# Kernel tuning notes

Hardware: AMD Instinct MI355X
Metric: run time of the kernel (lower is better)

Reference implementation:

```python
import jax, jax.numpy as jnp
import numpy as np
from math import ceil, log2

LEVELS = 10
DB4 = [-0.010597401785069032, 0.0328830116668852, 0.030841381835560764,
       -0.18703481171909309, -0.027983769416859854, 0.6308807679298589,
       0.7148465705529157, 0.2303778133088965]


def _convolve(x, f, transpose=False):
    # circular convolution (or correlation if transpose) via rFFT, filter zero-padded to signal length
    L = x.shape[-1]
    ra = jnp.fft.rfft(x)
    rb = jnp.fft.rfft(f, n=L)
    if transpose:
        rb = jnp.conj(rb)
    return jnp.fft.irfft(ra * rb, n=L)


def _compute_wavelet(s):
    # g = flip(s); g[1::2] *= -1
    g = jnp.flip(s, -1)
    sign = jnp.where(jnp.arange(g.shape[-1]) % 2 == 1, -1.0, 1.0).astype(g.dtype)
    return g * sign


def _compute_wavelet_synthesis(s):
    # g = flip(s); g[::2] *= -1
    g = jnp.flip(s, -1)
    sign = jnp.where(jnp.arange(g.shape[-1]) % 2 == 0, -1.0, 1.0).astype(g.dtype)
    return g * sign


def _hard_threshold(v, alpha, b_plus, b_minus):
    return v * (jax.nn.sigmoid(alpha * (v - b_plus)) + jax.nn.sigmoid(-alpha * (v + b_minus)))


def setup_inputs() -> dict:
    key = jax.random.key(0)
    x = jax.random.normal(key, (256, 65536), dtype=jnp.float32)
    filt = jnp.asarray(DB4, dtype=jnp.float32)
    scaling = jnp.tile(filt, (LEVELS, 1))       # (levels, 8)
    scaling_rec = jnp.tile(filt, (LEVELS, 1))   # (levels, 8)
    alpha = jnp.asarray(10.0, jnp.float32)
    b_plus = jnp.asarray(2.0, jnp.float32)
    b_minus = jnp.asarray(1.0, jnp.float32)
    return {"x": x, "scaling": scaling, "scaling_rec": scaling_rec,
            "alpha": alpha, "b_plus": b_plus, "b_minus": b_minus}


def reference(x, scaling, scaling_rec, alpha, b_plus, b_minus):
    n, input_length = x.shape
    desired = 2 ** ceil(log2(input_length))
    pad_l = (desired - input_length) // 2
    pad_r = ceil((desired - input_length) / 2)
    if pad_l or pad_r:
        x = jnp.pad(x, ((0, 0), (pad_l, pad_r)), mode="reflect")

    # forward lifting: note details = even_updated, new approximation = odd_updated
    approx = x
    coeffs = []
    for lvl in range(LEVELS):
        wav = _compute_wavelet(scaling_rec[lvl])
        even = approx[:, ::2]
        odd = approx[:, 1::2]
        odd_u = odd - _convolve(even, wav)
        even_u = even - _convolve(odd, scaling[lvl])
        coeffs.append(even_u)   # details
        approx = odd_u          # approximation
    coeffs.append(approx)

    filtered = [_hard_threshold(c, alpha, b_plus, b_minus) for c in coeffs]
    # l1_reg on a single tensor is sum(abs(.)) in the original code
    reg_loss = sum(jnp.sum(jnp.abs(c)) for c in filtered)

    # inverse lifting
    approx = filtered[-1]
    for lvl in reversed(range(LEVELS)):
        details = filtered[lvl]
        ws = _compute_wavelet_synthesis(scaling_rec[lvl])
        even, odd = details, approx
        even_rest = even + _convolve(odd, scaling[lvl], transpose=True)
        odd_rest = odd + _convolve(even, ws, transpose=True)
        # interleave even/odd back
        approx = jnp.stack([even_rest, odd_rest], axis=-1).reshape(even.shape[0], even.shape[1] * 2)

    return approx[:, pad_l:input_length + pad_l], reg_loss
```

## Files before the change

kernel.cpp:

```cpp
#include <hip/hip_runtime.h>

#define NROWS 256
#define ROWLEN 65536
#define TPB 1024
#define LOSS_IDX ((size_t)NROWS * (size_t)ROWLEN)

__device__ __forceinline__ int SW(int i) {
    return i ^ (((i >> 5) ^ (i >> 10)) & 31);
}

__device__ __forceinline__ float rfl(float x) {
    union { float f; int i; } u; u.f = x;
    u.i = __builtin_amdgcn_readfirstlane(u.i);
    return u.f;
}

__device__ __forceinline__ float sigm(float z) { return 1.0f / (1.0f + __expf(-z)); }

__device__ __forceinline__ float hthr(float v, float a, float bp, float bm) {
    return v * (sigm(a * (v - bp)) + sigm(-a * (v + bm)));
}

__device__ __forceinline__ void wave_sync() {
    __builtin_amdgcn_wave_barrier();
    __threadfence_block();
    __builtin_amdgcn_wave_barrier();
}

__device__ __forceinline__ void ldf_fwd(const float* sc, const float* rec, int lvl,
                                        float* sf, float* wv) {
    #pragma unroll
    for (int i = 0; i < 8; ++i) sf[i] = rfl(sc[lvl * 8 + i]);
    #pragma unroll
    for (int i = 0; i < 8; ++i) {
        float r = rfl(rec[lvl * 8 + 7 - i]);
        wv[i] = (i & 1) ? -r : r;
    }
}

__device__ __forceinline__ void ldf_rec(const float* sc, const float* rec, int lvl,
                                        float* sf, float* ws) {
    #pragma unroll
    for (int i = 0; i < 8; ++i) sf[i] = rfl(sc[lvl * 8 + i]);
    #pragma unroll
    for (int i = 0; i < 8; ++i) {
        float r = rfl(rec[lvl * 8 + 7 - i]);
        ws[i] = (i & 1) ? r : -r;
    }
}

template<int C, int S, int M, bool WAVE>
__device__ __forceinline__ void fwd_level(float* __restrict__ buf, int tid,
                                          const float* sf, const float* wv,
                                          float a, float bp, float bm, float& loss)
{
    const int c0 = tid * C;
    float ev[8], od[8];
    #pragma unroll
    for (int k = 0; k < 7; ++k) {
        int m = (c0 - 7 + k) & (M - 1);
        ev[k] = buf[SW(2 * m * S)];
        od[k] = buf[SW((2 * m + 1) * S)];
    }
    if constexpr (WAVE) wave_sync(); else __syncthreads();
    float ne = buf[SW(2 * c0 * S)];
    float no = buf[SW((2 * c0 + 1) * S)];
    #pragma unroll
    for (int j = 0; j < C; ++j) {
        const int n = c0 + j;
        ev[7] = ne; od[7] = no;
        if (j + 1 < C) {
            ne = buf[SW(2 * (n + 1) * S)];
            no = buf[SW((2 * (n + 1) + 1) * S)];
        }
        float ao = 0.f, ae = 0.f;
        #pragma unroll
        for (int k = 0; k < 8; ++k) {
            ao = fmaf(wv[k], ev[7 - k], ao);
            ae = fmaf(sf[k], od[7 - k], ae);
        }
        buf[SW(2 * n * S)] = od[7] - ao;
        float d = hthr(ev[7] - ae, a, bp, bm);
        loss += fabsf(d);
        buf[SW((2 * n + 1) * S)] = d;
        #pragma unroll
        for (int k = 0; k < 7; ++k) { ev[k] = ev[k + 1]; od[k] = od[k + 1]; }
    }
    if constexpr (WAVE) wave_sync(); else __syncthreads();
}

template<int C, int S, int M, bool WAVE>
__device__ __forceinline__ void rec_level(float* __restrict__ buf, int tid,
                                          const float* sf, const float* ws)
{
    const int c0 = tid * C;
    float ha[7], hd[7];
    #pragma unroll
    for (int k = 0; k < 7; ++k) {
        int m = (c0 + C + k) & (M - 1);
        ha[k] = buf[SW(2 * m * S)];
        hd[k] = buf[SW((2 * m + 1) * S)];
    }
    if constexpr (WAVE) wave_sync(); else __syncthreads();
    float ap[8], dt[8];
    #pragma unroll
    for (int k = 0; k < 8; ++k) {
        if (k < C) {
            ap[k] = buf[SW(2 * (c0 + k) * S)];
            dt[k] = buf[SW((2 * (c0 + k) + 1) * S)];
        } else {
            ap[k] = ha[k - C];
            dt[k] = hd[k - C];
        }
    }
    #pragma unroll
    for (int j = 0; j < C; ++j) {
        const int n = c0 + j;
        float er = 0.f, orr = 0.f;
        #pragma unroll
        for (int k = 0; k < 8; ++k) {
            er  = fmaf(sf[k], ap[k], er);
            orr = fmaf(ws[k], dt[k], orr);
        }
        er  += dt[0];
        orr += ap[0];
        buf[SW(2 * n * S)] = er;
        buf[SW((2 * n + 1) * S)] = orr;
        if (j + 1 < C) {
            #pragma unroll
            for (int k = 0; k < 7; ++k) { ap[k] = ap[k + 1]; dt[k] = dt[k + 1]; }
            const int nn = n + 8;
            if (j + 8 < C) {
                ap[7] = buf[SW(2 * nn * S)];
                dt[7] = buf[SW((2 * nn + 1) * S)];
            } else {
                ap[7] = ha[j + 8 - C];
                dt[7] = hd[j + 8 - C];
            }
        }
    }
    if constexpr (WAVE) wave_sync(); else __syncthreads();
}

__global__ __launch_bounds__(TPB)
__attribute__((amdgpu_num_vgpr(128), amdgpu_waves_per_eu(4, 4)))
void wavelet_vcycle_kernel(
    const float* __restrict__ x, const float* __restrict__ scaling,
    const float* __restrict__ scaling_rec, const float* __restrict__ pa,
    const float* __restrict__ pbp, const float* __restrict__ pbm,
    float* __restrict__ out)
{
    extern __shared__ float buf[];
    __shared__ float wb[16][8];
    __shared__ float lossbuf[16];
    const int tid  = threadIdx.x;
    const int lane = tid & 63;
    const int wv_id = tid >> 6;
    const int row = blockIdx.x;
    const float* xr = x + (size_t)row * ROWLEN;
    float* outr = out + (size_t)row * ROWLEN;
    const float a = rfl(pa[0]), bp = rfl(pbp[0]), bm = rfl(pbm[0]);
    float loss = 0.f;
    float sf[8], wv8[8];
    float det0[32];

    ldf_fwd(scaling, scaling_rec, 0, sf, wv8);
    {
        const int c0 = tid * 32;
        float ev[8], od[8];
        {
            const int b = 2 * c0;
            float4 h0 = *(const float4*)(xr + ((b - 16) & 65535));
            float4 h1 = *(const float4*)(xr + ((b - 12) & 65535));
            float4 h2 = *(const float4*)(xr + ((b -  8) & 65535));
            float4 h3 = *(const float4*)(xr + ((b -  4) & 65535));
            ev[0] = h0.z; od[0] = h0.w;
            ev[1] = h1.x; od[1] = h1.y; ev[2] = h1.z; od[2] = h1.w;
            ev[3] = h2.x; od[3] = h2.y; ev[4] = h2.z; od[4] = h2.w;
            ev[5] = h3.x; od[5] = h3.y; ev[6] = h3.z; od[6] = h3.w;
        }
        #pragma unroll
        for (int jj = 0; jj < 16; ++jj) {
            float4 v = *(const float4*)(xr + 2 * (c0 + 2 * jj));
            #pragma unroll
            for (int q = 0; q < 2; ++q) {
                const int j = 2 * jj + q;
                const int n = c0 + j;
                ev[7] = (q == 0) ? v.x : v.z;
                od[7] = (q == 0) ? v.y : v.w;
                float ao = 0.f, ae = 0.f;
                #pragma unroll
                for (int k = 0; k < 8; ++k) {
                    ao = fmaf(wv8[k], ev[7 - k], ao);
                    ae = fmaf(sf[k],  od[7 - k], ae);
                }
                buf[SW(n)] = od[7] - ao;
                float d = hthr(ev[7] - ae, a, bp, bm);
                loss += fabsf(d);
                det0[j] = d;
                #pragma unroll
                for (int k = 0; k < 7; ++k) { ev[k] = ev[k + 1]; od[k] = od[k + 1]; }
            }
        }
    }
    if (lane == 0) {
        #pragma unroll
        for (int k = 0; k < 7; ++k) wb[wv_id][k] = det0[k];
    }
    __syncthreads();

    ldf_fwd(scaling, scaling_rec, 1, sf, wv8); fwd_level<16, 1, 16384, false>(buf, tid, sf, wv8, a, bp, bm, loss);
    ldf_fwd(scaling, scaling_rec, 2, sf, wv8); fwd_level< 8, 2,  8192, false>(buf, tid, sf, wv8, a, bp, bm, loss);
    ldf_fwd(scaling, scaling_rec, 3, sf, wv8); fwd_level< 4, 4,  4096, false>(buf, tid, sf, wv8, a, bp, bm, loss);
    ldf_fwd(scaling, scaling_rec, 4, sf, wv8); fwd_level< 2, 8,  2048, false>(buf, tid, sf, wv8, a, bp, bm, loss);

    if (wv_id == 0) {
        ldf_fwd(scaling, scaling_rec, 5, sf, wv8); fwd_level<16,  16, 1024, true>(buf, lane, sf, wv8, a, bp, bm, loss);
        ldf_fwd(scaling, scaling_rec, 6, sf, wv8); fwd_level< 8,  32,  512, true>(buf, lane, sf, wv8, a, bp, bm, loss);
        ldf_fwd(scaling, scaling_rec, 7, sf, wv8); fwd_level< 4,  64,  256, true>(buf, lane, sf, wv8, a, bp, bm, loss);
        ldf_fwd(scaling, scaling_rec, 8, sf, wv8); fwd_level< 2, 128,  128, true>(buf, lane, sf, wv8, a, bp, bm, loss);
        ldf_fwd(scaling, scaling_rec, 9, sf, wv8); fwd_level< 1, 256,   64, true>(buf, lane, sf, wv8, a, bp, bm, loss);

        float v = buf[SW(lane * 512)];
        float f = hthr(v, a, bp, bm);
        loss += fabsf(f);
        buf[SW(lane * 512)] = f;
        wave_sync();

        ldf_rec(scaling, scaling_rec, 9, sf, wv8); rec_level< 1, 256,   64, true>(buf, lane, sf, wv8);
        ldf_rec(scaling, scaling_rec, 8, sf, wv8); rec_level< 2, 128,  128, true>(buf, lane, sf, wv8);
        ldf_rec(scaling, scaling_rec, 7, sf, wv8); rec_level< 4,  64,  256, true>(buf, lane, sf, wv8);
        ldf_rec(scaling, scaling_rec, 6, sf, wv8); rec_level< 8,  32,  512, true>(buf, lane, sf, wv8);
        ldf_rec(scaling, scaling_rec, 5, sf, wv8); rec_level<16,  16, 1024, true>(buf, lane, sf, wv8);
    }

    {
        float l = loss;
        #pragma unroll
        for (int off = 32; off > 0; off >>= 1) l += __shfl_down(l, off, 64);
        if (lane == 0) lossbuf[wv_id] = l;
    }
    __syncthreads();
    if (tid == 0) {
        float s = 0.f;
        #pragma unroll
        for (int w = 0; w < 16; ++w) s += lossbuf[w];
        atomicAdd(out + LOSS_IDX, s);
    }

    ldf_rec(scaling, scaling_rec, 4, sf, wv8); rec_level< 2, 8, 2048, false>(buf, tid, sf, wv8);
    ldf_rec(scaling, scaling_rec, 3, sf, wv8); rec_level< 4, 4, 4096, false>(buf, tid, sf, wv8);
    ldf_rec(scaling, scaling_rec, 2, sf, wv8); rec_level< 8, 2, 8192, false>(buf, tid, sf, wv8);
    ldf_rec(scaling, scaling_rec, 1, sf, wv8); rec_level<16, 1, 16384, false>(buf, tid, sf, wv8);

    {
        ldf_rec(scaling, scaling_rec, 0, sf, wv8);
        float h[7];
        #pragma unroll
        for (int k = 0; k < 7; ++k) h[k] = __shfl(det0[k], (lane + 1) & 63, 64);
        if (lane == 63) {
            #pragma unroll
            for (int k = 0; k < 7; ++k) h[k] = wb[(wv_id + 1) & 15][k];
        }
        #pragma unroll
        for (int p = 0; p < 2; ++p) {
            const int c0 = tid * 32 + p * 16;
            float ap[8];
            #pragma unroll
            for (int k = 0; k < 8; ++k) ap[k] = buf[SW((c0 + k) & 32767)];
            float e0 = 0.f, o0 = 0.f;
            #pragma unroll
            for (int j = 0; j < 16; ++j) {
                const int n = c0 + j;
                float er = 0.f, orr = 0.f;
                #pragma unroll
                for (int k = 0; k < 8; ++k) {
                    const int di = p * 16 + j + k;
                    float dv = (di < 32) ? det0[di] : h[di - 32];
                    er  = fmaf(sf[k],  ap[k], er);
                    orr = fmaf(wv8[k], dv,    orr);
                }
                const int d0i = p * 16 + j;
                float dvj = (d0i < 32) ? det0[d0i] : h[d0i - 32];
                er  += dvj;
                orr += ap[0];
                if ((j & 1) == 0) { e0 = er; o0 = orr; }
                else *(float4*)(outr + 2 * (n - 1)) = make_float4(e0, o0, er, orr);
                if (j < 15) {
                    #pragma unroll
                    for (int k = 0; k < 7; ++k) ap[k] = ap[k + 1];
                    ap[7] = buf[SW((n + 8) & 32767)];
                }
            }
        }
    }
}

extern "C" void kernel_launch(void* const* d_in, const int* in_sizes, int n_in,
                              void* d_out, int out_size, void* d_ws, size_t ws_size,
                              hipStream_t stream) {
    const float* x           = (const float*)d_in[0];
    const float* scaling     = (const float*)d_in[1];
    const float* scaling_rec = (const float*)d_in[2];
    const float* p_alpha     = (const float*)d_in[3];
    const float* p_bp        = (const float*)d_in[4];
    const float* p_bm        = (const float*)d_in[5];
    float* out = (float*)d_out;

    hipMemsetAsync(out + LOSS_IDX, 0, sizeof(float), stream);

    wavelet_vcycle_kernel<<<dim3(NROWS), dim3(TPB), 32768 * sizeof(float), stream>>>(
        x, scaling, scaling_rec, p_alpha, p_bp, p_bm, out);
}
```

Measured before the change: 85.54 us.

## Parallelize levels 5-6 across block, fuse threshold sigmoids, prefetch input loads

Moves wavelet levels 5 and 6 (forward and inverse) from a single wavefront to the whole 1024-thread block, with a guard for level 6 where only half the threads have work. This cuts the serial single-wave tail, at the cost of two extra block-wide barriers per direction. The hard threshold now combines both sigmoids into one expression with a single fast reciprocal, clamping the exponents to avoid overflow. The global input loads for level 0 are software-pipelined four float4s ahead.

New measurement: 73.49 us. 14.1% less time.

```diff
diff --git a/kernel.cpp b/kernel.cpp
--- a/kernel.cpp
+++ b/kernel.cpp
@@ -15,10 +15,13 @@
     return u.f;
 }
 
-__device__ __forceinline__ float sigm(float z) { return 1.0f / (1.0f + __expf(-z)); }
-
 __device__ __forceinline__ float hthr(float v, float a, float bp, float bm) {
-    return v * (sigm(a * (v - bp)) + sigm(-a * (v + bm)));
+    float e1 = __expf(fminf(-a * (v - bp), 80.f));
+    float e2 = __expf(fminf( a * (v + bm), 80.f));
+    float s  = e1 + e2;
+    float num = 2.f + s;
+    float den = fmaf(e1, e2, 1.f + s);
+    return v * num * __builtin_amdgcn_rcpf(den);
 }
 
 __device__ __forceinline__ void wave_sync() {
@@ -49,93 +52,103 @@
     }
 }
 
-template<int C, int S, int M, bool WAVE>
+template<int C, int S, int M, bool WAVE, bool GUARD>
 __device__ __forceinline__ void fwd_level(float* __restrict__ buf, int tid,
                                           const float* sf, const float* wv,
                                           float a, float bp, float bm, float& loss)
 {
+    const bool act = !GUARD || (tid * C < M);
     const int c0 = tid * C;
     float ev[8], od[8];
-    #pragma unroll
-    for (int k = 0; k < 7; ++k) {
-        int m = (c0 - 7 + k) & (M - 1);
-        ev[k] = buf[SW(2 * m * S)];
-        od[k] = buf[SW((2 * m + 1) * S)];
+    if (act) {
+        #pragma unroll
+        for (int k = 0; k < 7; ++k) {
+            int m = (c0 - 7 + k) & (M - 1);
+            ev[k] = buf[SW(2 * m * S)];
+            od[k] = buf[SW((2 * m + 1) * S)];
+        }
     }
     if constexpr (WAVE) wave_sync(); else __syncthreads();
-    float ne = buf[SW(2 * c0 * S)];
-    float no = buf[SW((2 * c0 + 1) * S)];
-    #pragma unroll
-    for (int j = 0; j < C; ++j) {
-        const int n = c0 + j;
-        ev[7] = ne; od[7] = no;
-        if (j + 1 < C) {
-            ne = buf[SW(2 * (n + 1) * S)];
-            no = buf[SW((2 * (n + 1) + 1) * S)];
-        }
-        float ao = 0.f, ae = 0.f;
-        #pragma unroll
-        for (int k = 0; k < 8; ++k) {
-            ao = fmaf(wv[k], ev[7 - k], ao);
-            ae = fmaf(sf[k], od[7 - k], ae);
-        }
-        buf[SW(2 * n * S)] = od[7] - ao;
-        float d = hthr(ev[7] - ae, a, bp, bm);
-        loss += fabsf(d);
-        buf[SW((2 * n + 1) * S)] = d;
-        #pragma unroll
-        for (int k = 0; k < 7; ++k) { ev[k] = ev[k + 1]; od[k] = od[k + 1]; }
+    if (act) {
+        float ne = buf[SW(2 * c0 * S)];
+        float no = buf[SW((2 * c0 + 1) * S)];
+        #pragma unroll
+        for (int j = 0; j < C; ++j) {
+            const int n = c0 + j;
+            ev[7] = ne; od[7] = no;
+            if (j + 1 < C) {
+                ne = buf[SW(2 * (n + 1) * S)];
+                no = buf[SW((2 * (n + 1) + 1) * S)];
+            }
+            float ao = 0.f, ae = 0.f;
+            #pragma unroll
+            for (int k = 0; k < 8; ++k) {
+                ao = fmaf(wv[k], ev[7 - k], ao);
+                ae = fmaf(sf[k], od[7 - k], ae);
+            }
+            buf[SW(2 * n * S)] = od[7] - ao;
+            float d = hthr(ev[7] - ae, a, bp, bm);
+            loss += fabsf(d);
+            buf[SW((2 * n + 1) * S)] = d;
+            #pragma unroll
+            for (int k = 0; k < 7; ++k) { ev[k] = ev[k + 1]; od[k] = od[k + 1]; }
+        }
     }
     if constexpr (WAVE) wave_sync(); else __syncthreads();
 }
 
-template<int C, int S, int M, bool WAVE>
+template<int C, int S, int M, bool WAVE, bool GUARD>
 __device__ __forceinline__ void rec_level(float* __restrict__ buf, int tid,
                                           const float* sf, const float* ws)
 {
+    const bool act = !GUARD || (tid * C < M);
     const int c0 = tid * C;
     float ha[7], hd[7];
-    #pragma unroll
-    for (int k = 0; k < 7; ++k) {
-        int m = (c0 + C + k) & (M - 1);
-        ha[k] = buf[SW(2 * m * S)];
-        hd[k] = buf[SW((2 * m + 1) * S)];
+    if (act) {
+        #pragma unroll
+        for (int k = 0; k < 7; ++k) {
+            int m = (c0 + C + k) & (M - 1);
+            ha[k] = buf[SW(2 * m * S)];
+            hd[k] = buf[SW((2 * m + 1) * S)];
+        }
     }
     if constexpr (WAVE) wave_sync(); else __syncthreads();
-    float ap[8], dt[8];
-    #pragma unroll
-    for (int k = 0; k < 8; ++k) {
-        if (k < C) {
-            ap[k] = buf[SW(2 * (c0 + k) * S)];
-            dt[k] = buf[SW((2 * (c0 + k) + 1) * S)];
-        } else {
-            ap[k] = ha[k - C];
-            dt[k] = hd[k - C];
-        }
-    }
-    #pragma unroll
-    for (int j = 0; j < C; ++j) {
-        const int n = c0 + j;
-        float er = 0.f, orr = 0.f;
+    if (act) {
+        float ap[8], dt[8];
         #pragma unroll
         for (int k = 0; k < 8; ++k) {
-            er  = fmaf(sf[k], ap[k], er);
-            orr = fmaf(ws[k], dt[k], orr);
-        }
-        er  += dt[0];
-        orr += ap[0];
-        buf[SW(2 * n * S)] = er;
-        buf[SW((2 * n + 1) * S)] = orr;
-        if (j + 1 < C) {
-            #pragma unroll
-            for (int k = 0; k < 7; ++k) { ap[k] = ap[k + 1]; dt[k] = dt[k + 1]; }
-            const int nn = n + 8;
-            if (j + 8 < C) {
-                ap[7] = buf[SW(2 * nn * S)];
-                dt[7] = buf[SW((2 * nn + 1) * S)];
+            if (k < C) {
+                ap[k] = buf[SW(2 * (c0 + k) * S)];
+                dt[k] = buf[SW((2 * (c0 + k) + 1) * S)];
             } else {
-                ap[7] = ha[j + 8 - C];
-                dt[7] = hd[j + 8 - C];
+                ap[k] = ha[k - C];
+                dt[k] = hd[k - C];
+            }
+        }
+        #pragma unroll
+        for (int j = 0; j < C; ++j) {
+            const int n = c0 + j;
+            float er = 0.f, orr = 0.f;
+            #pragma unroll
+            for (int k = 0; k < 8; ++k) {
+                er  = fmaf(sf[k], ap[k], er);
+                orr = fmaf(ws[k], dt[k], orr);
+            }
+            er  += dt[0];
+            orr += ap[0];
+            buf[SW(2 * n * S)] = er;
+            buf[SW((2 * n + 1) * S)] = orr;
+            if (j + 1 < C) {
+                #pragma unroll
+                for (int k = 0; k < 7; ++k) { ap[k] = ap[k + 1]; dt[k] = dt[k + 1]; }
+                const int nn = n + 8;
+                if (j + 8 < C) {
+                    ap[7] = buf[SW(2 * nn * S)];
+                    dt[7] = buf[SW((2 * nn + 1) * S)];
+                } else {
+                    ap[7] = ha[j + 8 - C];
+                    dt[7] = hd[j + 8 - C];
+                }
             }
         }
     }
@@ -179,13 +192,18 @@
             ev[3] = h2.x; od[3] = h2.y; ev[4] = h2.z; od[4] = h2.w;
             ev[5] = h3.x; od[5] = h3.y; ev[6] = h3.z; od[6] = h3.w;
         }
+        float4 x4[4];
+        #pragma unroll
+        for (int jj = 0; jj < 4; ++jj)
+            x4[jj] = *(const float4*)(xr + 2 * (c0 + 2 * jj));
         #pragma unroll
         for (int jj = 0; jj < 16; ++jj) {
-            float4 v = *(const float4*)(xr + 2 * (c0 + 2 * jj));
+            float4 v = x4[jj & 3];
+            if (jj + 4 < 16)
+                x4[jj & 3] = *(const float4*)(xr + 2 * (c0 + 2 * (jj + 4)));
             #pragma unroll
             for (int q = 0; q < 2; ++q) {
                 const int j = 2 * jj + q;
-                const int n = c0 + j;
                 ev[7] = (q == 0) ? v.x : v.z;
                 od[7] = (q == 0) ? v.y : v.w;
                 float ao = 0.f, ae = 0.f;
@@ -194,7 +212,7 @@
                     ao = fmaf(wv8[k], ev[7 - k], ao);
                     ae = fmaf(sf[k],  od[7 - k], ae);
                 }
-                buf[SW(n)] = od[7] - ao;
+                buf[SW(c0 + j)] = od[7] - ao;
                 float d = hthr(ev[7] - ae, a, bp, bm);
                 loss += fabsf(d);
                 det0[j] = d;
@@ -209,17 +227,17 @@
     }
     __syncthreads();
 
-    ldf_fwd(scaling, scaling_rec, 1, sf, wv8); fwd_level<16, 1, 16384, false>(buf, tid, sf, wv8, a, bp, bm, loss);
-    ldf_fwd(scaling, scaling_rec, 2, sf, wv8); fwd_level< 8, 2,  8192, false>(buf, tid, sf, wv8, a, bp, bm, loss);
-    ldf_fwd(scaling, scaling_rec, 3, sf, wv8); fwd_level< 4, 4,  4096, false>(buf, tid, sf, wv8, a, bp, bm, loss);
-    ldf_fwd(scaling, scaling_rec, 4, sf, wv8); fwd_level< 2, 8,  2048, false>(buf, tid, sf, wv8, a, bp, bm, loss);
+    ldf_fwd(scaling, scaling_rec, 1, sf, wv8); fwd_level<16, 1, 16384, false, false>(buf, tid, sf, wv8, a, bp, bm, loss);
+    ldf_fwd(scaling, scaling_rec, 2, sf, wv8); fwd_level< 8, 2,  8192, false, false>(buf, tid, sf, wv8, a, bp, bm, loss);
+    ldf_fwd(scaling, scaling_rec, 3, sf, wv8); fwd_level< 4, 4,  4096, false, false>(buf, tid, sf, wv8, a, bp, bm, loss);
+    ldf_fwd(scaling, scaling_rec, 4, sf, wv8); fwd_level< 2, 8,  2048, false, false>(buf, tid, sf, wv8, a, bp, bm, loss);
+    ldf_fwd(scaling, scaling_rec, 5, sf, wv8); fwd_level< 1, 16, 1024, false, false>(buf, tid, sf, wv8, a, bp, bm, loss);
+    ldf_fwd(scaling, scaling_rec, 6, sf, wv8); fwd_level< 1, 32,  512, false, true >(buf, tid, sf, wv8, a, bp, bm, loss);
 
     if (wv_id == 0) {
-        ldf_fwd(scaling, scaling_rec, 5, sf, wv8); fwd_level<16,  16, 1024, true>(buf, lane, sf, wv8, a, bp, bm, loss);
-        ldf_fwd(scaling, scaling_rec, 6, sf, wv8); fwd_level< 8,  32,  512, true>(buf, lane, sf, wv8, a, bp, bm, loss);
-        ldf_fwd(scaling, scaling_rec, 7, sf, wv8); fwd_level< 4,  64,  256, true>(buf, lane, sf, wv8, a, bp, bm, loss);
-        ldf_fwd(scaling, scaling_rec, 8, sf, wv8); fwd_level< 2, 128,  128, true>(buf, lane, sf, wv8, a, bp, bm, loss);
-        ldf_fwd(scaling, scaling_rec, 9, sf, wv8); fwd_level< 1, 256,   64, true>(buf, lane, sf, wv8, a, bp, bm, loss);
+        ldf_fwd(scaling, scaling_rec, 7, sf, wv8); fwd_level< 4,  64, 256, true, false>(buf, lane, sf, wv8, a, bp, bm, loss);
+        ldf_fwd(scaling, scaling_rec, 8, sf, wv8); fwd_level< 2, 128, 128, true, false>(buf, lane, sf, wv8, a, bp, bm, loss);
+        ldf_fwd(scaling, scaling_rec, 9, sf, wv8); fwd_level< 1, 256,  64, true, false>(buf, lane, sf, wv8, a, bp, bm, loss);
 
         float v = buf[SW(lane * 512)];
         float f = hthr(v, a, bp, bm);
@@ -227,11 +245,9 @@
         buf[SW(lane * 512)] = f;
         wave_sync();
 
-        ldf_rec(scaling, scaling_rec, 9, sf, wv8); rec_level< 1, 256,   64, true>(buf, lane, sf, wv8);
-        ldf_rec(scaling, scaling_rec, 8, sf, wv8); rec_level< 2, 128,  128, true>(buf, lane, sf, wv8);
-        ldf_rec(scaling, scaling_rec, 7, sf, wv8); rec_level< 4,  64,  256, true>(buf, lane, sf, wv8);
-        ldf_rec(scaling, scaling_rec, 6, sf, wv8); rec_level< 8,  32,  512, true>(buf, lane, sf, wv8);
-        ldf_rec(scaling, scaling_rec, 5, sf, wv8); rec_level<16,  16, 1024, true>(buf, lane, sf, wv8);
+        ldf_rec(scaling, scaling_rec, 9, sf, wv8); rec_level< 1, 256,  64, true, false>(buf, lane, sf, wv8);
+        ldf_rec(scaling, scaling_rec, 8, sf, wv8); rec_level< 2, 128, 128, true, false>(buf, lane, sf, wv8);
+        ldf_rec(scaling, scaling_rec, 7, sf, wv8); rec_level< 4,  64, 256, true, false>(buf, lane, sf, wv8);
     }
 
     {
@@ -248,10 +264,12 @@
         atomicAdd(out + LOSS_IDX, s);
     }
 
-    ldf_rec(scaling, scaling_rec, 4, sf, wv8); rec_level< 2, 8, 2048, false>(buf, tid, sf, wv8);
-    ldf_rec(scaling, scaling_rec, 3, sf, wv8); rec_level< 4, 4, 4096, false>(buf, tid, sf, wv8);
-    ldf_rec(scaling, scaling_rec, 2, sf, wv8); rec_level< 8, 2, 8192, false>(buf, tid, sf, wv8);
-    ldf_rec(scaling, scaling_rec, 1, sf, wv8); rec_level<16, 1, 16384, false>(buf, tid, sf, wv8);
+    ldf_rec(scaling, scaling_rec, 6, sf, wv8); rec_level< 1, 32,  512, false, true >(buf, tid, sf, wv8);
+    ldf_rec(scaling, scaling_rec, 5, sf, wv8); rec_level< 1, 16, 1024, false, false>(buf, tid, sf, wv8);
+    ldf_rec(scaling, scaling_rec, 4, sf, wv8); rec_level< 2, 8,  2048, false, false>(buf, tid, sf, wv8);
+    ldf_rec(scaling, scaling_rec, 3, sf, wv8); rec_level< 4, 4,  4096, false, false>(buf, tid, sf, wv8);
+    ldf_rec(scaling, scaling_rec, 2, sf, wv8); rec_level< 8, 2,  8192, false, false>(buf, tid, sf, wv8);
+    ldf_rec(scaling, scaling_rec, 1, sf, wv8); rec_level<16, 1, 16384, false, false>(buf, tid, sf, wv8);
 
     {
         ldf_rec(scaling, scaling_rec, 0, sf, wv8);
```
